# Optimization experiments

Hardware: AMD Instinct MI355X
Metric: run time of the kernel (lower is better)

The kernel has to match this reference:

```python
import jax, jax.numpy as jnp
import numpy as np

SR = 48000.0
STAB_EPS = 1e-3
BS = 32
N_FRAMES = 128
N_SAMPLES = 65536


def setup_inputs() -> dict:
    key = jax.random.key(0)
    ks = jax.random.split(key, 8)
    f0_hz = jax.random.uniform(ks[0], (BS,), minval=50.0, maxval=500.0)
    note_on_duration = jax.random.uniform(ks[1], (BS,), minval=0.3, maxval=1.0)
    phase = jax.random.uniform(ks[2], (BS,), minval=-np.pi, maxval=np.pi)
    logits = jax.random.normal(ks[3], (BS, N_FRAMES, 5))
    osc_shape = jax.random.uniform(ks[4], (BS,))
    osc_gain = jax.random.uniform(ks[5], (BS,), minval=0.5, maxval=1.0)
    dist_gain = jax.random.uniform(ks[6], (BS,), minval=1.0, maxval=4.0)
    learned_alpha = jax.random.uniform(ks[7], (BS,), minval=0.5, maxval=3.0)
    return dict(f0_hz=f0_hz, note_on_duration=note_on_duration, phase=phase,
                logits=logits, osc_shape=osc_shape, osc_gain=osc_gain,
                dist_gain=dist_gain, learned_alpha=learned_alpha,
                n_samples=N_SAMPLES)


def lin_interp_dim1(x, n_out):
    """Linear interpolation along dim 1 with align_corners=True. x: (bs, n_in, c)."""
    n_in = x.shape[1]
    pos = jnp.linspace(0.0, n_in - 1.0, n_out)
    i0 = jnp.floor(pos).astype(jnp.int32)
    i1 = jnp.minimum(i0 + 1, n_in - 1)
    frac = (pos - i0.astype(x.dtype))[None, :, None]
    return x[:, i0] * (1.0 - frac) + x[:, i1] * frac


def square_saw_vco(f0_hz, osc_shape, n_samples, phase):
    """torchsynth-style square/saw morph oscillator. f0_hz, osc_shape, phase: (bs,)."""
    f0 = f0_hz[:, None]                                   # (bs, 1)
    inc = jnp.broadcast_to(f0 / SR, (f0.shape[0], n_samples))
    arg = 2.0 * jnp.pi * jnp.cumsum(inc, axis=1) + phase[:, None]
    partials = 12000.0 / (f0 * jnp.log10(f0))
    square = jnp.tanh(jnp.pi * partials * jnp.sin(arg) / 2.0)
    s = osc_shape[:, None]
    return (1.0 - s / 2.0) * square * (1.0 + s * jnp.cos(arg / 2.0))


def exp_decay_env(alpha, note_on_duration, n_samples):
    t = jnp.arange(n_samples, dtype=jnp.float32) / SR     # (n,)
    ramp = jnp.clip(1.0 - t[None, :] / note_on_duration[:, None], STAB_EPS, 1.0)
    env = ramp ** alpha[:, None]
    return jnp.where(t[None, :] <= note_on_duration[:, None], env, 0.0)


def logits_to_a_coeff_triangle(a_logits):
    """Map 2 logits to a stable biquad denominator (a1, a2) inside the stability triangle."""
    stab = 1.0 - STAB_EPS
    a1 = 2.0 * jnp.tanh(a_logits[..., 0]) * stab
    a1_abs = jnp.abs(a1)
    a2 = ((2.0 - a1_abs) * jnp.tanh(a_logits[..., 1]) * stab + a1_abs) / 2.0
    return jnp.stack([a1, a2], axis=-1)


def sample_wise_lpc(x, a):
    """Time-varying all-pole order-2: y[t] = x[t] - a1[t]*y[t-1] - a2[t]*y[t-2].
    x: (bs, n), a: (bs, n, 2). Sequential lax.scan over time."""
    def step(carry, inp):
        y1, y2 = carry
        xt, a1, a2 = inp
        y = xt - a1 * y1 - a2 * y2
        return (y, y1), y
    z = jnp.zeros(x.shape[0], dtype=x.dtype)
    xs = (x.T, a[..., 0].T, a[..., 1].T)                  # time-major
    _, ys = jax.lax.scan(step, (z, z), xs)
    return ys.T


def time_varying_fir(x, b):
    """y[t] = b0[t]*x[t] + b1[t]*x[t-1] + b2[t]*x[t-2], zero initial state."""
    x1 = jnp.pad(x, ((0, 0), (1, 0)))[:, :-1]
    x2 = jnp.pad(x, ((0, 0), (2, 0)))[:, :-2]
    return b[..., 0] * x + b[..., 1] * x1 + b[..., 2] * x2


def reference(f0_hz, note_on_duration, phase, logits, osc_shape, osc_gain,
              dist_gain, learned_alpha, n_samples):
    # --- oscillator + envelope ---
    dry = square_saw_vco(f0_hz, osc_shape, n_samples, phase)
    dry = dry * osc_gain[:, None]
    envelope = exp_decay_env(learned_alpha, note_on_duration, n_samples)
    dry = dry * envelope
    # --- coefficients (interp_logits=False: map to coeffs at frame rate, then upsample) ---
    a_coeff = logits_to_a_coeff_triangle(logits[..., :2])   # (bs, n_frames, 2)
    b_coeff = logits[..., 2:]                                # (bs, n_frames, 3)
    a_coeff = lin_interp_dim1(a_coeff, n_samples)            # (bs, n, 2)
    b_coeff = lin_interp_dim1(b_coeff, n_samples)            # (bs, n, 3)
    # --- time-varying biquad: all-pole recursion then FIR ---
    y_a = sample_wise_lpc(dry, a_coeff)
    y_ab = time_varying_fir(y_a, b_coeff)
    # --- distortion ---
    wet = jnp.tanh(y_ab * dist_gain[:, None])
    a0 = jnp.ones_like(a_coeff[:, :, 0])
    a_coeff3 = jnp.stack([a0, a_coeff[:, :, 0], a_coeff[:, :, 1]], axis=2)
    return (dry, wet, envelope, y_ab, a_coeff3, b_coeff, y_a)
```

## Files before the change

### kernel.cpp

```cpp
#include <hip/hip_runtime.h>
#include <cmath>

#define DI __device__ __forceinline__

constexpr int BS = 32;
constexpr int NS = 65536;
constexpr int NF = 128;
constexpr int S  = 4;
constexpr int TB = 256;
constexpr int SAMP = TB * S;
constexpr int NC = NS / SAMP;
constexpr size_t U = (size_t)BS * NS;
constexpr double PI_D = 3.14159265358979323846;
constexpr float STAB = 0.999f;

struct M6 { float a, b, c, d, u, v; };

DI M6 comp(const M6& R, const M6& L) {
    M6 o;
    o.a = fmaf(R.a, L.a, R.b * L.c);
    o.b = fmaf(R.a, L.b, R.b * L.d);
    o.c = fmaf(R.c, L.a, R.d * L.c);
    o.d = fmaf(R.c, L.b, R.d * L.d);
    o.u = fmaf(R.a, L.u, fmaf(R.b, L.v, R.u));
    o.v = fmaf(R.c, L.u, fmaf(R.d, L.v, R.v));
    return o;
}

DI void stepL(M6& A, float a1, float a2, float x) {
    float na = fmaf(-a1, A.a, -a2 * A.c);
    float nb = fmaf(-a1, A.b, -a2 * A.d);
    float nu = fmaf(-a1, A.u, fmaf(-a2, A.v, x));
    A.c = A.a; A.d = A.b; A.v = A.u;
    A.a = na;  A.b = nb;  A.u = nu;
}

DI void wave_scan6(M6& s, int lane) {
    #pragma unroll
    for (int d = 1; d < 64; d <<= 1) {
        M6 o;
        o.a = __shfl_up(s.a, d, 64); o.b = __shfl_up(s.b, d, 64);
        o.c = __shfl_up(s.c, d, 64); o.d = __shfl_up(s.d, d, 64);
        o.u = __shfl_up(s.u, d, 64); o.v = __shfl_up(s.v, d, 64);
        M6 t = comp(s, o);
        bool p = lane >= d;
        s.a = p ? t.a : s.a; s.b = p ? t.b : s.b; s.c = p ? t.c : s.c;
        s.d = p ? t.d : s.d; s.u = p ? t.u : s.u; s.v = p ? t.v : s.v;
    }
}

DI M6 ld6(const float* p) { M6 m; m.a=p[0]; m.b=p[1]; m.c=p[2]; m.d=p[3]; m.u=p[4]; m.v=p[5]; return m; }
DI void st6(float* p, const M6& m) { p[0]=m.a; p[1]=m.b; p[2]=m.c; p[3]=m.d; p[4]=m.u; p[5]=m.v; }

DI void ipos(int t, int& i0, int& i1, float& fr) {
    double pos = (double)t * (127.0 / 65535.0);
    int p0 = (int)pos;
    i0 = p0;
    i1 = (p0 + 1 > 127) ? 127 : p0 + 1;
    fr = (float)(pos - (double)p0);
}

DI float fast_tanh(float x) {
    float e = __expf(2.0f * x);
    return 1.0f - 2.0f / (e + 1.0f);
}

DI void stage_frames(const float* __restrict__ logits, int b, int F, int tid,
                     float (*sfa)[2], float (*sfb)[3]) {
    if (tid < 4) {
        int fidx = F + tid; if (fidx > 127) fidx = 127;
        const float* L = logits + (size_t)(b * NF + fidx) * 5;
        float a1 = 2.0f * tanhf(L[0]) * STAB;
        float aa = fabsf(a1);
        float a2 = ((2.0f - aa) * tanhf(L[1]) * STAB + aa) * 0.5f;
        sfa[tid][0] = a1; sfa[tid][1] = a2;
        sfb[tid][0] = L[2]; sfb[tid][1] = L[3]; sfb[tid][2] = L[4];
    }
}

DI void interp4(int t0, int F, const float (*sfa)[2], const float (*sfb)[3],
                float* a1v, float* a2v, float* b0v, float* b1v, float* b2v) {
    #pragma unroll
    for (int k = 0; k < S; k++) {
        int i0, i1; float fr;
        ipos(t0 + k, i0, i1, fr);
        float w0 = 1.0f - fr;
        int l0 = i0 - F, l1 = i1 - F;
        a1v[k] = sfa[l0][0] * w0 + sfa[l1][0] * fr;
        a2v[k] = sfa[l0][1] * w0 + sfa[l1][1] * fr;
        b0v[k] = sfb[l0][0] * w0 + sfb[l1][0] * fr;
        b1v[k] = sfb[l0][1] * w0 + sfb[l1][1] * fr;
        b2v[k] = sfb[l0][2] * w0 + sfb[l1][2] * fr;
    }
}

__global__ __launch_bounds__(TB) void k_osc(
    const float* __restrict__ f0_hz, const float* __restrict__ note_dur,
    const float* __restrict__ phase, const float* __restrict__ logits,
    const float* __restrict__ osc_shape, const float* __restrict__ osc_gain,
    const float* __restrict__ alpha,
    float* __restrict__ ws_chunk, float* __restrict__ out) {
    __shared__ float sfa[4][2], sfb[4][3], wt[4][6];
    const int bid = blockIdx.x;
    const int b = bid / NC, c = bid % NC;
    const int tid = threadIdx.x;
    const int t0 = c * SAMP + tid * S;
    const size_t g0 = (size_t)b * NS + t0;
    const int F = (int)((double)(c * SAMP) * (127.0 / 65535.0));

    stage_frames(logits, b, F, tid, sfa, sfb);

    const float f0 = f0_hz[b];
    const float ph = phase[b];
    const float sh = osc_shape[b];
    const float gn = osc_gain[b];
    const float dur = note_dur[b];
    const float al = alpha[b];
    const double inc = (double)f0 / 48000.0;
    const float partials = 12000.0f / (f0 * __log10f(f0));

    float x[S], env4[S];
    #pragma unroll
    for (int k = 0; k < S; k++) {
        int t = t0 + k;
        double cum = (double)(t + 1) * inc;
        double uu = cum - 2.0 * floor(cum * 0.5);
        float theta = (float)(PI_D * uu + 0.5 * (double)ph);
        float sn, cs;
        __sincosf(theta, &sn, &cs);
        float sq = fast_tanh(1.57079632679f * partials * (2.0f * sn * cs));
        float dry0 = (1.0f - 0.5f * sh) * sq * (1.0f + sh * cs);
        float tsec = (float)t * (1.0f / 48000.0f);
        float env = 0.0f;
        if (tsec <= dur) {
            float ramp = 1.0f - tsec / dur;
            ramp = ramp < 0.001f ? 0.001f : (ramp > 1.0f ? 1.0f : ramp);
            env = __expf(al * __logf(ramp));
        }
        env4[k] = env;
        x[k] = dry0 * gn * env;
    }
    __syncthreads();

    float a1v[S], a2v[S], b0v[S], b1v[S], b2v[S];
    interp4(t0, F, sfa, sfb, a1v, a2v, b0v, b1v, b2v);

    *(float4*)&out[g0]         = make_float4(x[0], x[1], x[2], x[3]);
    *(float4*)&out[2 * U + g0] = make_float4(env4[0], env4[1], env4[2], env4[3]);
    float* a3 = out + 4 * U + g0 * 3;
    *(float4*)&a3[0] = make_float4(1.0f, a1v[0], a2v[0], 1.0f);
    *(float4*)&a3[4] = make_float4(a1v[1], a2v[1], 1.0f, a1v[2]);
    *(float4*)&a3[8] = make_float4(a2v[2], 1.0f, a1v[3], a2v[3]);
    float* bc = out + 7 * U + g0 * 3;
    *(float4*)&bc[0] = make_float4(b0v[0], b1v[0], b2v[0], b0v[1]);
    *(float4*)&bc[4] = make_float4(b1v[1], b2v[1], b0v[2], b1v[2]);
    *(float4*)&bc[8] = make_float4(b2v[2], b0v[3], b1v[3], b2v[3]);

    M6 A; A.a = -a1v[0]; A.b = -a2v[0]; A.c = 1.0f; A.d = 0.0f; A.u = x[0]; A.v = 0.0f;
    #pragma unroll
    for (int k = 1; k < S; k++) stepL(A, a1v[k], a2v[k], x[k]);

    const int lane = tid & 63, w = tid >> 6;
    wave_scan6(A, lane);
    if (lane == 63) st6(wt[w], A);
    __syncthreads();
    if (tid == TB - 1) {
        M6 p = ld6(wt[0]);
        p = comp(ld6(wt[1]), p);
        p = comp(ld6(wt[2]), p);
        M6 tot = comp(A, p);
        st6(ws_chunk + ((size_t)b * NC + c) * 6, tot);
    }
}

__global__ __launch_bounds__(TB) void k_iir(
    const float* __restrict__ logits, const float* __restrict__ dist_gain,
    const float* __restrict__ ws_chunk, float* __restrict__ out) {
    __shared__ float sfa[4][2], sfb[4][3], wt[4][6], sv[NC][2];
    const int bid = blockIdx.x;
    const int b = bid / NC, c = bid % NC;
    const int tid = threadIdx.x;
    const int t0 = c * SAMP + tid * S;
    const size_t g0 = (size_t)b * NS + t0;
    const int F = (int)((double)(c * SAMP) * (127.0 / 65535.0));

    stage_frames(logits, b, F, tid, sfa, sfb);

    if (tid < NC) {
        M6 cs = ld6(ws_chunk + ((size_t)b * NC + tid) * 6);
        wave_scan6(cs, tid);
        sv[tid][0] = cs.u; sv[tid][1] = cs.v;
    }

    float4 xv = *(const float4*)&out[g0];
    float x[S] = {xv.x, xv.y, xv.z, xv.w};

    __syncthreads();
    const float s0 = c ? sv[c - 1][0] : 0.0f;
    const float s1 = c ? sv[c - 1][1] : 0.0f;

    float a1v[S], a2v[S], b0v[S], b1v[S], b2v[S];
    interp4(t0, F, sfa, sfb, a1v, a2v, b0v, b1v, b2v);

    M6 A; A.a = -a1v[0]; A.b = -a2v[0]; A.c = 1.0f; A.d = 0.0f; A.u = x[0]; A.v = 0.0f;
    #pragma unroll
    for (int k = 1; k < S; k++) stepL(A, a1v[k], a2v[k], x[k]);

    const int lane = tid & 63, w = tid >> 6;
    wave_scan6(A, lane);
    if (lane == 63) st6(wt[w], A);
    __syncthreads();

    M6 P; P.a = 1.f; P.b = 0.f; P.c = 0.f; P.d = 1.f; P.u = 0.f; P.v = 0.f;
    for (int i = 0; i < w; i++) P = comp(ld6(wt[i]), P);
    M6 prev;
    prev.a = __shfl_up(A.a, 1, 64); prev.b = __shfl_up(A.b, 1, 64);
    prev.c = __shfl_up(A.c, 1, 64); prev.d = __shfl_up(A.d, 1, 64);
    prev.u = __shfl_up(A.u, 1, 64); prev.v = __shfl_up(A.v, 1, 64);
    M6 E = (lane == 0) ? P : comp(prev, P);

    float y1 = fmaf(E.a, s0, fmaf(E.b, s1, E.u));
    float y2 = fmaf(E.c, s0, fmaf(E.d, s1, E.v));
    const float ys0 = y1, ys1 = y2;

    float y[S];
    #pragma unroll
    for (int k = 0; k < S; k++) {
        y[k] = fmaf(-a1v[k], y1, fmaf(-a2v[k], y2, x[k]));
        y2 = y1; y1 = y[k];
    }

    const float dg = dist_gain[b];
    float yab[S], wet[S];
    #pragma unroll
    for (int k = 0; k < S; k++) {
        float ym1 = (k >= 1) ? y[k - 1] : ys0;
        float ym2 = (k >= 2) ? y[k - 2] : ((k == 1) ? ys0 : ys1);
        yab[k] = b0v[k] * y[k] + b1v[k] * ym1 + b2v[k] * ym2;
        wet[k] = fast_tanh(yab[k] * dg);
    }

    *(float4*)&out[U + g0]      = make_float4(wet[0], wet[1], wet[2], wet[3]);
    *(float4*)&out[3 * U + g0]  = make_float4(yab[0], yab[1], yab[2], yab[3]);
    *(float4*)&out[10 * U + g0] = make_float4(y[0], y[1], y[2], y[3]);
}

extern "C" void kernel_launch(void* const* d_in, const int* in_sizes, int n_in,
                              void* d_out, int out_size, void* d_ws, size_t ws_size,
                              hipStream_t stream) {
    const float* f0   = (const float*)d_in[0];
    const float* dur  = (const float*)d_in[1];
    const float* ph   = (const float*)d_in[2];
    const float* lg   = (const float*)d_in[3];
    const float* shp  = (const float*)d_in[4];
    const float* gn   = (const float*)d_in[5];
    const float* dist = (const float*)d_in[6];
    const float* alp  = (const float*)d_in[7];
    float* out = (float*)d_out;
    float* ws_chunk = (float*)d_ws;

    k_osc<<<BS * NC, TB, 0, stream>>>(f0, dur, ph, lg, shp, gn, alp, ws_chunk, out);
    k_iir<<<BS * NC, TB, 0, stream>>>(lg, dist, ws_chunk, out);
}
```

Measured before the change: 131.9 us.

## Fuse oscillator and IIR passes into one cooperative kernel with grid sync

Merges the two kernels into a single cooperative launch that keeps the dry signal in registers across a grid-wide barrier, so it is not re-read and the phase-1 chunk scan is not recomputed. Each thread now handles 16 samples instead of 4, which cuts the grid to 512 blocks. Phase is stepped incrementally in float instead of being recomputed in double per sample, and the interpolation position moves to float. In exchange it adds host-side occupancy queries on every launch, depends on the grid-sync cost, and changes precision slightly; a two-kernel fallback covers the case where cooperative launch is unavailable.

```diff
diff --git a/kernel.cpp b/kernel.cpp
--- a/kernel.cpp
+++ b/kernel.cpp
@@ -1,18 +1,24 @@
 #include <hip/hip_runtime.h>
+#include <hip/hip_cooperative_groups.h>
 #include <cmath>
 
+namespace cg = cooperative_groups;
 #define DI __device__ __forceinline__
 
 constexpr int BS = 32;
 constexpr int NS = 65536;
 constexpr int NF = 128;
-constexpr int S  = 4;
 constexpr int TB = 256;
+constexpr int S  = 16;
+constexpr int G  = 8;
 constexpr int SAMP = TB * S;
 constexpr int NC = NS / SAMP;
+constexpr int GRID = BS * NC;
+constexpr int NFR = 10;
 constexpr size_t U = (size_t)BS * NS;
 constexpr double PI_D = 3.14159265358979323846;
 constexpr float STAB = 0.999f;
+constexpr float CPOS = 127.0f / 65535.0f;
 
 struct M6 { float a, b, c, d, u, v; };
 
@@ -35,9 +41,10 @@
     A.a = na;  A.b = nb;  A.u = nu;
 }
 
+template <int W>
 DI void wave_scan6(M6& s, int lane) {
     #pragma unroll
-    for (int d = 1; d < 64; d <<= 1) {
+    for (int d = 1; d < W; d <<= 1) {
         M6 o;
         o.a = __shfl_up(s.a, d, 64); o.b = __shfl_up(s.b, d, 64);
         o.c = __shfl_up(s.c, d, 64); o.d = __shfl_up(s.d, d, 64);
@@ -52,14 +59,6 @@
 DI M6 ld6(const float* p) { M6 m; m.a=p[0]; m.b=p[1]; m.c=p[2]; m.d=p[3]; m.u=p[4]; m.v=p[5]; return m; }
 DI void st6(float* p, const M6& m) { p[0]=m.a; p[1]=m.b; p[2]=m.c; p[3]=m.d; p[4]=m.u; p[5]=m.v; }
 
-DI void ipos(int t, int& i0, int& i1, float& fr) {
-    double pos = (double)t * (127.0 / 65535.0);
-    int p0 = (int)pos;
-    i0 = p0;
-    i1 = (p0 + 1 > 127) ? 127 : p0 + 1;
-    fr = (float)(pos - (double)p0);
-}
-
 DI float fast_tanh(float x) {
     float e = __expf(2.0f * x);
     return 1.0f - 2.0f / (e + 1.0f);
@@ -67,7 +66,7 @@
 
 DI void stage_frames(const float* __restrict__ logits, int b, int F, int tid,
                      float (*sfa)[2], float (*sfb)[3]) {
-    if (tid < 4) {
+    if (tid < NFR) {
         int fidx = F + tid; if (fidx > 127) fidx = 127;
         const float* L = logits + (size_t)(b * NF + fidx) * 5;
         float a1 = 2.0f * tanhf(L[0]) * STAB;
@@ -78,171 +77,218 @@
     }
 }
 
-DI void interp4(int t0, int F, const float (*sfa)[2], const float (*sfb)[3],
-                float* a1v, float* a2v, float* b0v, float* b1v, float* b2v) {
-    #pragma unroll
-    for (int k = 0; k < S; k++) {
-        int i0, i1; float fr;
-        ipos(t0 + k, i0, i1, fr);
-        float w0 = 1.0f - fr;
-        int l0 = i0 - F, l1 = i1 - F;
-        a1v[k] = sfa[l0][0] * w0 + sfa[l1][0] * fr;
-        a2v[k] = sfa[l0][1] * w0 + sfa[l1][1] * fr;
-        b0v[k] = sfb[l0][0] * w0 + sfb[l1][0] * fr;
-        b1v[k] = sfb[l0][1] * w0 + sfb[l1][1] * fr;
-        b2v[k] = sfb[l0][2] * w0 + sfb[l1][2] * fr;
-    }
-}
-
-__global__ __launch_bounds__(TB) void k_osc(
+DI void interp_at(int t, int F, const float (*sfa)[2], const float (*sfb)[3],
+                  float& a1, float& a2, float& b0, float& b1, float& b2) {
+    float pos = (float)t * CPOS;
+    int i0 = (int)pos;
+    int i1 = (i0 + 1 > 127) ? 127 : i0 + 1;
+    float fr = pos - (float)i0, w0 = 1.0f - fr;
+    int l0 = i0 - F, l1 = i1 - F;
+    a1 = sfa[l0][0] * w0 + sfa[l1][0] * fr;
+    a2 = sfa[l0][1] * w0 + sfa[l1][1] * fr;
+    b0 = sfb[l0][0] * w0 + sfb[l1][0] * fr;
+    b1 = sfb[l0][1] * w0 + sfb[l1][1] * fr;
+    b2 = sfb[l0][2] * w0 + sfb[l1][2] * fr;
+}
+
+DI M6 block_scan_E(M6 A, float (*wt)[6], int tid, float* publish) {
+    const int lane = tid & 63, w = tid >> 6;
+    wave_scan6<64>(A, lane);
+    if (lane == 63) st6(wt[w], A);
+    __syncthreads();
+    M6 P; P.a = 1.f; P.b = 0.f; P.c = 0.f; P.d = 1.f; P.u = 0.f; P.v = 0.f;
+    for (int i = 0; i < w; i++) P = comp(ld6(wt[i]), P);
+    if (publish && tid == TB - 1) st6(publish, comp(A, P));
+    M6 prev;
+    prev.a = __shfl_up(A.a, 1, 64); prev.b = __shfl_up(A.b, 1, 64);
+    prev.c = __shfl_up(A.c, 1, 64); prev.d = __shfl_up(A.d, 1, 64);
+    prev.u = __shfl_up(A.u, 1, 64); prev.v = __shfl_up(A.v, 1, 64);
+    return (lane == 0) ? P : comp(prev, P);
+}
+
+DI void cross_scan(const float* __restrict__ ws_chunk, int b, int tid,
+                   float (*sv)[2]) {
+    if (tid < 64) {
+        M6 cs;
+        if (tid < NC) cs = ld6(ws_chunk + ((size_t)b * NC + tid) * 6);
+        else { cs.a = 1.f; cs.b = 0.f; cs.c = 0.f; cs.d = 1.f; cs.u = 0.f; cs.v = 0.f; }
+        wave_scan6<NC>(cs, tid);
+        if (tid < NC) { sv[tid][0] = cs.u; sv[tid][1] = cs.v; }
+    }
+}
+
+DI M6 dev_phase1(int b, int c, int tid,
+    const float* __restrict__ f0_hz, const float* __restrict__ note_dur,
+    const float* __restrict__ phase, const float* __restrict__ logits,
+    const float* __restrict__ osc_shape, const float* __restrict__ osc_gain,
+    const float* __restrict__ alpha,
+    float* __restrict__ ws_chunk, float* __restrict__ out,
+    float (*sfa)[2], float (*sfb)[3], float (*wt)[6], float* x16) {
+    const int t0 = c * SAMP + tid * S;
+    const size_t g0 = (size_t)b * NS + t0;
+    const int F = (int)((float)(c * SAMP) * CPOS);
+
+    stage_frames(logits, b, F, tid, sfa, sfb);
+
+    const float f0 = f0_hz[b], ph = phase[b], sh = osc_shape[b];
+    const float gn = osc_gain[b], dur = note_dur[b], al = alpha[b];
+    const double inc = (double)f0 / 48000.0;
+    const float partials = 12000.0f / (f0 * __log10f(f0));
+    const double cum0 = (double)(t0 + 1) * inc;
+    const double uu0 = cum0 - 2.0 * floor(cum0 * 0.5);
+    const float theta0 = (float)(PI_D * uu0 + 0.5 * (double)ph);
+    const float dth = (float)(PI_D * inc);
+
+    __syncthreads();
+
+    M6 A;
+    #pragma unroll
+    for (int h = 0; h < 2; h++) {
+        float xv[G], ev[G], a1s[G], a2s[G], b0s[G], b1s[G], b2s[G];
+        #pragma unroll
+        for (int k = 0; k < G; k++) {
+            int idx = h * G + k, t = t0 + idx;
+            float theta = theta0 + (float)idx * dth;
+            float sn, cs;
+            __sincosf(theta, &sn, &cs);
+            float sq = fast_tanh(1.57079632679f * partials * (2.0f * sn * cs));
+            float dry0 = (1.0f - 0.5f * sh) * sq * (1.0f + sh * cs);
+            float tsec = (float)t * (1.0f / 48000.0f);
+            float env = 0.0f;
+            if (tsec <= dur) {
+                float ramp = 1.0f - tsec / dur;
+                ramp = ramp < 0.001f ? 0.001f : (ramp > 1.0f ? 1.0f : ramp);
+                env = __expf(al * __logf(ramp));
+            }
+            ev[k] = env;
+            float x = dry0 * gn * env;
+            xv[k] = x; x16[idx] = x;
+            float a1, a2, b0, b1, b2;
+            interp_at(t, F, sfa, sfb, a1, a2, b0, b1, b2);
+            a1s[k] = a1; a2s[k] = a2; b0s[k] = b0; b1s[k] = b1; b2s[k] = b2;
+            if (h == 0 && k == 0) { A.a = -a1; A.b = -a2; A.c = 1.f; A.d = 0.f; A.u = x; A.v = 0.f; }
+            else stepL(A, a1, a2, x);
+        }
+        const size_t gh = g0 + h * G;
+        *(float4*)&out[gh]             = make_float4(xv[0], xv[1], xv[2], xv[3]);
+        *(float4*)&out[gh + 4]         = make_float4(xv[4], xv[5], xv[6], xv[7]);
+        *(float4*)&out[2 * U + gh]     = make_float4(ev[0], ev[1], ev[2], ev[3]);
+        *(float4*)&out[2 * U + gh + 4] = make_float4(ev[4], ev[5], ev[6], ev[7]);
+        float* a3 = out + 4 * U + gh * 3;
+        *(float4*)&a3[0]  = make_float4(1.0f, a1s[0], a2s[0], 1.0f);
+        *(float4*)&a3[4]  = make_float4(a1s[1], a2s[1], 1.0f, a1s[2]);
+        *(float4*)&a3[8]  = make_float4(a2s[2], 1.0f, a1s[3], a2s[3]);
+        *(float4*)&a3[12] = make_float4(1.0f, a1s[4], a2s[4], 1.0f);
+        *(float4*)&a3[16] = make_float4(a1s[5], a2s[5], 1.0f, a1s[6]);
+        *(float4*)&a3[20] = make_float4(a2s[6], 1.0f, a1s[7], a2s[7]);
+        float* bc = out + 7 * U + gh * 3;
+        *(float4*)&bc[0]  = make_float4(b0s[0], b1s[0], b2s[0], b0s[1]);
+        *(float4*)&bc[4]  = make_float4(b1s[1], b2s[1], b0s[2], b1s[2]);
+        *(float4*)&bc[8]  = make_float4(b2s[2], b0s[3], b1s[3], b2s[3]);
+        *(float4*)&bc[12] = make_float4(b0s[4], b1s[4], b2s[4], b0s[5]);
+        *(float4*)&bc[16] = make_float4(b1s[5], b2s[5], b0s[6], b1s[6]);
+        *(float4*)&bc[20] = make_float4(b2s[6], b0s[7], b1s[7], b2s[7]);
+    }
+    return block_scan_E(A, wt, tid, ws_chunk + ((size_t)b * NC + c) * 6);
+}
+
+DI void dev_phase2(int b, int c, int tid, const float* x16, M6 E,
+                   float s0, float s1, const float (*sfa)[2],
+                   const float (*sfb)[3], float dg, float* __restrict__ out) {
+    const int t0 = c * SAMP + tid * S;
+    const size_t g0 = (size_t)b * NS + t0;
+    const int F = (int)((float)(c * SAMP) * CPOS);
+    float y1 = fmaf(E.a, s0, fmaf(E.b, s1, E.u));
+    float y2 = fmaf(E.c, s0, fmaf(E.d, s1, E.v));
+    #pragma unroll
+    for (int h = 0; h < 2; h++) {
+        float yv[G], yabv[G], wetv[G];
+        #pragma unroll
+        for (int k = 0; k < G; k++) {
+            int idx = h * G + k, t = t0 + idx;
+            float a1, a2, b0, b1, b2;
+            interp_at(t, F, sfa, sfb, a1, a2, b0, b1, b2);
+            float yn = fmaf(-a1, y1, fmaf(-a2, y2, x16[idx]));
+            float yab = b0 * yn + b1 * y1 + b2 * y2;
+            yv[k] = yn; yabv[k] = yab; wetv[k] = fast_tanh(yab * dg);
+            y2 = y1; y1 = yn;
+        }
+        const size_t gh = g0 + h * G;
+        *(float4*)&out[U + gh]          = make_float4(wetv[0], wetv[1], wetv[2], wetv[3]);
+        *(float4*)&out[U + gh + 4]      = make_float4(wetv[4], wetv[5], wetv[6], wetv[7]);
+        *(float4*)&out[3 * U + gh]      = make_float4(yabv[0], yabv[1], yabv[2], yabv[3]);
+        *(float4*)&out[3 * U + gh + 4]  = make_float4(yabv[4], yabv[5], yabv[6], yabv[7]);
+        *(float4*)&out[10 * U + gh]     = make_float4(yv[0], yv[1], yv[2], yv[3]);
+        *(float4*)&out[10 * U + gh + 4] = make_float4(yv[4], yv[5], yv[6], yv[7]);
+    }
+}
+
+__global__ __launch_bounds__(TB, 4) void k_fused(
+    const float* __restrict__ f0_hz, const float* __restrict__ note_dur,
+    const float* __restrict__ phase, const float* __restrict__ logits,
+    const float* __restrict__ osc_shape, const float* __restrict__ osc_gain,
+    const float* __restrict__ dist_gain, const float* __restrict__ alpha,
+    float* __restrict__ ws_chunk, float* __restrict__ out) {
+    __shared__ float sfa[NFR][2], sfb[NFR][3], wt[4][6], sv[NC][2];
+    const int bid = blockIdx.x, b = bid / NC, c = bid % NC, tid = threadIdx.x;
+    float x16[S];
+    M6 E = dev_phase1(b, c, tid, f0_hz, note_dur, phase, logits, osc_shape,
+                      osc_gain, alpha, ws_chunk, out, sfa, sfb, wt, x16);
+    __threadfence();
+    cg::this_grid().sync();
+    cross_scan(ws_chunk, b, tid, sv);
+    __syncthreads();
+    const float s0 = c ? sv[c - 1][0] : 0.0f;
+    const float s1 = c ? sv[c - 1][1] : 0.0f;
+    dev_phase2(b, c, tid, x16, E, s0, s1, sfa, sfb, dist_gain[b], out);
+}
+
+__global__ __launch_bounds__(TB) void k_p1(
     const float* __restrict__ f0_hz, const float* __restrict__ note_dur,
     const float* __restrict__ phase, const float* __restrict__ logits,
     const float* __restrict__ osc_shape, const float* __restrict__ osc_gain,
     const float* __restrict__ alpha,
     float* __restrict__ ws_chunk, float* __restrict__ out) {
-    __shared__ float sfa[4][2], sfb[4][3], wt[4][6];
-    const int bid = blockIdx.x;
-    const int b = bid / NC, c = bid % NC;
-    const int tid = threadIdx.x;
+    __shared__ float sfa[NFR][2], sfb[NFR][3], wt[4][6];
+    const int bid = blockIdx.x, b = bid / NC, c = bid % NC, tid = threadIdx.x;
+    float x16[S];
+    (void)dev_phase1(b, c, tid, f0_hz, note_dur, phase, logits, osc_shape,
+                     osc_gain, alpha, ws_chunk, out, sfa, sfb, wt, x16);
+}
+
+__global__ __launch_bounds__(TB) void k_p2(
+    const float* __restrict__ logits, const float* __restrict__ dist_gain,
+    const float* __restrict__ ws_chunk, float* __restrict__ out) {
+    __shared__ float sfa[NFR][2], sfb[NFR][3], wt[4][6], sv[NC][2];
+    const int bid = blockIdx.x, b = bid / NC, c = bid % NC, tid = threadIdx.x;
     const int t0 = c * SAMP + tid * S;
     const size_t g0 = (size_t)b * NS + t0;
-    const int F = (int)((double)(c * SAMP) * (127.0 / 65535.0));
+    const int F = (int)((float)(c * SAMP) * CPOS);
 
     stage_frames(logits, b, F, tid, sfa, sfb);
-
-    const float f0 = f0_hz[b];
-    const float ph = phase[b];
-    const float sh = osc_shape[b];
-    const float gn = osc_gain[b];
-    const float dur = note_dur[b];
-    const float al = alpha[b];
-    const double inc = (double)f0 / 48000.0;
-    const float partials = 12000.0f / (f0 * __log10f(f0));
-
-    float x[S], env4[S];
+    cross_scan(ws_chunk, b, tid, sv);
+
+    float x16[S];
+    #pragma unroll
+    for (int q = 0; q < S / 4; q++) {
+        float4 v = *(const float4*)&out[g0 + q * 4];
+        x16[q * 4 + 0] = v.x; x16[q * 4 + 1] = v.y;
+        x16[q * 4 + 2] = v.z; x16[q * 4 + 3] = v.w;
+    }
+    __syncthreads();
+
+    M6 A;
     #pragma unroll
     for (int k = 0; k < S; k++) {
-        int t = t0 + k;
-        double cum = (double)(t + 1) * inc;
-        double uu = cum - 2.0 * floor(cum * 0.5);
-        float theta = (float)(PI_D * uu + 0.5 * (double)ph);
-        float sn, cs;
-        __sincosf(theta, &sn, &cs);
-        float sq = fast_tanh(1.57079632679f * partials * (2.0f * sn * cs));
-        float dry0 = (1.0f - 0.5f * sh) * sq * (1.0f + sh * cs);
-        float tsec = (float)t * (1.0f / 48000.0f);
-        float env = 0.0f;
-        if (tsec <= dur) {
-            float ramp = 1.0f - tsec / dur;
-            ramp = ramp < 0.001f ? 0.001f : (ramp > 1.0f ? 1.0f : ramp);
-            env = __expf(al * __logf(ramp));
-        }
-        env4[k] = env;
-        x[k] = dry0 * gn * env;
-    }
-    __syncthreads();
-
-    float a1v[S], a2v[S], b0v[S], b1v[S], b2v[S];
-    interp4(t0, F, sfa, sfb, a1v, a2v, b0v, b1v, b2v);
-
-    *(float4*)&out[g0]         = make_float4(x[0], x[1], x[2], x[3]);
-    *(float4*)&out[2 * U + g0] = make_float4(env4[0], env4[1], env4[2], env4[3]);
-    float* a3 = out + 4 * U + g0 * 3;
-    *(float4*)&a3[0] = make_float4(1.0f, a1v[0], a2v[0], 1.0f);
-    *(float4*)&a3[4] = make_float4(a1v[1], a2v[1], 1.0f, a1v[2]);
-    *(float4*)&a3[8] = make_float4(a2v[2], 1.0f, a1v[3], a2v[3]);
-    float* bc = out + 7 * U + g0 * 3;
-    *(float4*)&bc[0] = make_float4(b0v[0], b1v[0], b2v[0], b0v[1]);
-    *(float4*)&bc[4] = make_float4(b1v[1], b2v[1], b0v[2], b1v[2]);
-    *(float4*)&bc[8] = make_float4(b2v[2], b0v[3], b1v[3], b2v[3]);
-
-    M6 A; A.a = -a1v[0]; A.b = -a2v[0]; A.c = 1.0f; A.d = 0.0f; A.u = x[0]; A.v = 0.0f;
-    #pragma unroll
-    for (int k = 1; k < S; k++) stepL(A, a1v[k], a2v[k], x[k]);
-
-    const int lane = tid & 63, w = tid >> 6;
-    wave_scan6(A, lane);
-    if (lane == 63) st6(wt[w], A);
-    __syncthreads();
-    if (tid == TB - 1) {
-        M6 p = ld6(wt[0]);
-        p = comp(ld6(wt[1]), p);
-        p = comp(ld6(wt[2]), p);
-        M6 tot = comp(A, p);
-        st6(ws_chunk + ((size_t)b * NC + c) * 6, tot);
-    }
-}
-
-__global__ __launch_bounds__(TB) void k_iir(
-    const float* __restrict__ logits, const float* __restrict__ dist_gain,
-    const float* __restrict__ ws_chunk, float* __restrict__ out) {
-    __shared__ float sfa[4][2], sfb[4][3], wt[4][6], sv[NC][2];
-    const int bid = blockIdx.x;
-    const int b = bid / NC, c = bid % NC;
-    const int tid = threadIdx.x;
-    const int t0 = c * SAMP + tid * S;
-    const size_t g0 = (size_t)b * NS + t0;
-    const int F = (int)((double)(c * SAMP) * (127.0 / 65535.0));
-
-    stage_frames(logits, b, F, tid, sfa, sfb);
-
-    if (tid < NC) {
-        M6 cs = ld6(ws_chunk + ((size_t)b * NC + tid) * 6);
-        wave_scan6(cs, tid);
-        sv[tid][0] = cs.u; sv[tid][1] = cs.v;
-    }
-
-    float4 xv = *(const float4*)&out[g0];
-    float x[S] = {xv.x, xv.y, xv.z, xv.w};
-
-    __syncthreads();
+        float a1, a2, b0, b1, b2;
+        interp_at(t0 + k, F, sfa, sfb, a1, a2, b0, b1, b2);
+        if (k == 0) { A.a = -a1; A.b = -a2; A.c = 1.f; A.d = 0.f; A.u = x16[0]; A.v = 0.f; }
+        else stepL(A, a1, a2, x16[k]);
+    }
+    M6 E = block_scan_E(A, wt, tid, nullptr);
     const float s0 = c ? sv[c - 1][0] : 0.0f;
     const float s1 = c ? sv[c - 1][1] : 0.0f;
-
-    float a1v[S], a2v[S], b0v[S], b1v[S], b2v[S];
-    interp4(t0, F, sfa, sfb, a1v, a2v, b0v, b1v, b2v);
-
-    M6 A; A.a = -a1v[0]; A.b = -a2v[0]; A.c = 1.0f; A.d = 0.0f; A.u = x[0]; A.v = 0.0f;
-    #pragma unroll
-    for (int k = 1; k < S; k++) stepL(A, a1v[k], a2v[k], x[k]);
-
-    const int lane = tid & 63, w = tid >> 6;
-    wave_scan6(A, lane);
-    if (lane == 63) st6(wt[w], A);
-    __syncthreads();
-
-    M6 P; P.a = 1.f; P.b = 0.f; P.c = 0.f; P.d = 1.f; P.u = 0.f; P.v = 0.f;
-    for (int i = 0; i < w; i++) P = comp(ld6(wt[i]), P);
-    M6 prev;
-    prev.a = __shfl_up(A.a, 1, 64); prev.b = __shfl_up(A.b, 1, 64);
-    prev.c = __shfl_up(A.c, 1, 64); prev.d = __shfl_up(A.d, 1, 64);
-    prev.u = __shfl_up(A.u, 1, 64); prev.v = __shfl_up(A.v, 1, 64);
-    M6 E = (lane == 0) ? P : comp(prev, P);
-
-    float y1 = fmaf(E.a, s0, fmaf(E.b, s1, E.u));
-    float y2 = fmaf(E.c, s0, fmaf(E.d, s1, E.v));
-    const float ys0 = y1, ys1 = y2;
-
-    float y[S];
-    #pragma unroll
-    for (int k = 0; k < S; k++) {
-        y[k] = fmaf(-a1v[k], y1, fmaf(-a2v[k], y2, x[k]));
-        y2 = y1; y1 = y[k];
-    }
-
-    const float dg = dist_gain[b];
-    float yab[S], wet[S];
-    #pragma unroll
-    for (int k = 0; k < S; k++) {
-        float ym1 = (k >= 1) ? y[k - 1] : ys0;
-        float ym2 = (k >= 2) ? y[k - 2] : ((k == 1) ? ys0 : ys1);
-        yab[k] = b0v[k] * y[k] + b1v[k] * ym1 + b2v[k] * ym2;
-        wet[k] = fast_tanh(yab[k] * dg);
-    }
-
-    *(float4*)&out[U + g0]      = make_float4(wet[0], wet[1], wet[2], wet[3]);
-    *(float4*)&out[3 * U + g0]  = make_float4(yab[0], yab[1], yab[2], yab[3]);
-    *(float4*)&out[10 * U + g0] = make_float4(y[0], y[1], y[2], y[3]);
+    dev_phase2(b, c, tid, x16, E, s0, s1, sfa, sfb, dist_gain[b], out);
 }
 
 extern "C" void kernel_launch(void* const* d_in, const int* in_sizes, int n_in,
@@ -259,6 +305,22 @@
     float* out = (float*)d_out;
     float* ws_chunk = (float*)d_ws;
 
-    k_osc<<<BS * NC, TB, 0, stream>>>(f0, dur, ph, lg, shp, gn, alp, ws_chunk, out);
-    k_iir<<<BS * NC, TB, 0, stream>>>(lg, dist, ws_chunk, out);
-}
+    int dev = 0, numCU = 0, maxb = 0;
+    (void)hipGetDevice(&dev);
+    (void)hipDeviceGetAttribute(&numCU, hipDeviceAttributeMultiprocessorCount, dev);
+    hipError_t qe = hipOccupancyMaxActiveBlocksPerMultiprocessor(
+        &maxb, (const void*)k_fused, TB, 0);
+    bool ok = (qe == hipSuccess) && numCU > 0 && (long)maxb * numCU >= GRID;
+    if (ok) {
+        void* args[] = {(void*)&f0, (void*)&dur, (void*)&ph, (void*)&lg,
+                        (void*)&shp, (void*)&gn, (void*)&dist, (void*)&alp,
+                        (void*)&ws_chunk, (void*)&out};
+        if (hipLaunchCooperativeKernel((const void*)k_fused, dim3(GRID), dim3(TB),
+                                       args, 0, stream) != hipSuccess)
+            ok = false;
+    }
+    if (!ok) {
+        k_p1<<<GRID, TB, 0, stream>>>(f0, dur, ph, lg, shp, gn, alp, ws_chunk, out);
+        k_p2<<<GRID, TB, 0, stream>>>(lg, dist, ws_chunk, out);
+    }
+}
```

After: 310.8 us. 2.36x slower.
